# Kernel tuning notes

Measured on AMD Instinct MI355X. Metric: run time of the kernel, lower is better.

The kernel has to match this reference:

```python
import jax, jax.numpy as jnp
import numpy as np

B, C, H, W = 32, 512, 32, 32
D = C // 8

def setup_inputs() -> dict:
    key = jax.random.key(0)
    ks = jax.random.split(key, 5)
    return {
        "x": jax.random.normal(ks[0], (B, C, H, W), dtype=jnp.float32),
        "w1": jax.random.normal(ks[1], (D, C), dtype=jnp.float32) * (1.0 / np.sqrt(C)),
        "b1": jax.random.normal(ks[2], (D,), dtype=jnp.float32) * 0.01,
        "w2": jax.random.normal(ks[3], (C, C), dtype=jnp.float32) * (1.0 / np.sqrt(C)),
        "b2": jax.random.normal(ks[4], (C,), dtype=jnp.float32) * 0.01,
    }

def reference(x, w1, b1, w2, b2):
    b, c, h, w = x.shape
    n = h * w
    xf = x.reshape(b, c, n)                                   # [B,C,N]
    # 1x1 convs == channel-mixing GEMMs; conv1 is shared for q and k
    qk = jnp.einsum('bcn,dc->bdn', xf, w1) + b1[None, :, None]  # [B,D,N]
    v = jnp.einsum('bcn,oc->bon', xf, w2) + b2[None, :, None]   # [B,C,N]
    q = qk.transpose(0, 2, 1)                                 # [B,N,D]
    attn = jax.nn.softmax(jnp.einsum('bnd,bdm->bnm', q, qk), axis=-1)  # [B,N,N]
    out = jnp.einsum('bnm,bcm->bnc', attn, v)                 # [B,N,C]
    # Faithful quirk: original views [B,N,C] directly as [B,C,H,W] (no transpose)
    return x + out.reshape(b, c, h, w)
```

## Files before the change

### kernel.cpp

```cpp
#include <hip/hip_runtime.h>
#include <hip/hip_bf16.h>
#include <math.h>

#define B_ 32
#define C_ 512
#define N_ 1024
#define D_ 64
#define OPAD 640

typedef __attribute__((ext_vector_type(4))) float f32x4;
typedef __attribute__((ext_vector_type(4))) float float4v;
typedef __attribute__((ext_vector_type(8))) __bf16 bf16x8;

#define MFMA16(a, b, c) __builtin_amdgcn_mfma_f32_16x16x32_bf16((a), (b), (c), 0, 0, 0)

__device__ inline void load_lds16(const void* g, void* l) {
    __builtin_amdgcn_global_load_lds(
        (const __attribute__((address_space(1))) void*)g,
        (__attribute__((address_space(3))) void*)l, 16, 0, 0);
}

__global__ __launch_bounds__(256) void k_transpose_cast(
        const float* __restrict__ x,
        const float* __restrict__ w1, const float* __restrict__ w2,
        __hip_bfloat16* __restrict__ xT, __hip_bfloat16* __restrict__ Wbf) {
    __shared__ float tile[64][68];
    int b = blockIdx.z;
    int n0 = blockIdx.x * 64;
    int c0 = blockIdx.y * 64;
    int t = threadIdx.x;

    int lid = blockIdx.x + 16 * blockIdx.y + 128 * blockIdx.z;
    if (lid < 160) {
        int base = lid * 2048 + t * 8;
        int m = base >> 9, k = base & 511;
        alignas(16) __hip_bfloat16 wtmp[8];
        if (m < D_ + C_) {
            const float* s = (m < D_) ? w1 + (size_t)m * C_ + k
                                      : w2 + (size_t)(m - D_) * C_ + k;
            float4v a = *(const float4v*)s;
            float4v c = *(const float4v*)(s + 4);
            wtmp[0] = __float2bfloat16(a.x); wtmp[1] = __float2bfloat16(a.y);
            wtmp[2] = __float2bfloat16(a.z); wtmp[3] = __float2bfloat16(a.w);
            wtmp[4] = __float2bfloat16(c.x); wtmp[5] = __float2bfloat16(c.y);
            wtmp[6] = __float2bfloat16(c.z); wtmp[7] = __float2bfloat16(c.w);
        } else {
#pragma unroll
            for (int j = 0; j < 8; j++) wtmp[j] = __float2bfloat16(0.0f);
        }
        *(bf16x8*)(Wbf + base) = *(bf16x8*)wtmp;
    }

    const float* xb = x + (size_t)b * (C_ * N_);
#pragma unroll
    for (int i = 0; i < 4; i++) {
        int c = i * 16 + (t >> 4);
        int nc = (t & 15) * 4;
        *(float4v*)&tile[c][nc] =
            *(const float4v*)(xb + (size_t)(c0 + c) * N_ + n0 + nc);
    }
    __syncthreads();
    __hip_bfloat16* xTb = xT + (size_t)b * (N_ * C_);
#pragma unroll
    for (int i = 0; i < 2; i++) {
        int n = i * 32 + (t >> 3);
        int cs = (t & 7) * 8;
        alignas(16) __hip_bfloat16 tmp[8];
#pragma unroll
        for (int j = 0; j < 8; j++)
            tmp[j] = __float2bfloat16(tile[cs + j][n]);
        *(bf16x8*)(xTb + (size_t)(n0 + n) * C_ + c0 + cs) = *(bf16x8*)tmp;
    }
}

__global__ __launch_bounds__(256) void k_gemm_qkv(
        const __hip_bfloat16* __restrict__ Wbf,
        const __hip_bfloat16* __restrict__ xT,
        const float* __restrict__ b1, const float* __restrict__ b2,
        __hip_bfloat16* __restrict__ qkT, __hip_bfloat16* __restrict__ v) {
    __shared__ __hip_bfloat16 AB[2][2][128 * 64];
    __hip_bfloat16* epi = &AB[0][0][0];
    int b = blockIdx.x;
    int t = threadIdx.x;
    int wave = t >> 6, lane = t & 63, lr = lane & 15, quad = lane >> 4;
    int wm = wave >> 1, wn = wave & 1;
    int m_blk = blockIdx.z * 128;
    int n_blk = blockIdx.y * 128;
    const __hip_bfloat16* xTb = xT + (size_t)b * (N_ * C_);

#pragma unroll
    for (int i = 0; i < 4; i++) {
        int id = i * 256 + t;
        int r = id >> 3, cx = id & 7, gc = cx ^ (r & 7);
        load_lds16(Wbf + (size_t)(m_blk + r) * C_ + gc * 8, &AB[0][0][id * 8]);
        load_lds16(xTb + (size_t)(n_blk + r) * C_ + gc * 8, &AB[0][1][id * 8]);
    }
    __syncthreads();

    f32x4 acc[4][4] = {};
    for (int tt = 0; tt < 8; tt++) {
        const __hip_bfloat16* As = AB[tt & 1][0];
        const __hip_bfloat16* Bs = AB[tt & 1][1];
        if (tt < 7) {
            int kk = (tt + 1) * 64;
            __hip_bfloat16* An = AB[(tt + 1) & 1][0];
            __hip_bfloat16* Bn = AB[(tt + 1) & 1][1];
#pragma unroll
            for (int i = 0; i < 4; i++) {
                int id = i * 256 + t;
                int r = id >> 3, cx = id & 7, gc = cx ^ (r & 7);
                load_lds16(Wbf + (size_t)(m_blk + r) * C_ + kk + gc * 8, &An[id * 8]);
                load_lds16(xTb + (size_t)(n_blk + r) * C_ + kk + gc * 8, &Bn[id * 8]);
            }
        }
#pragma unroll
        for (int h = 0; h < 2; h++) {
            bf16x8 af[4], bfr[4];
#pragma unroll
            for (int i = 0; i < 4; i++) {
                int ra = wm * 64 + i * 16 + lr;
                int rb = wn * 64 + i * 16 + lr;
                int q = h * 4 + quad;
                af[i]  = *(const bf16x8*)&As[ra * 64 + (q ^ (lr & 7)) * 8];
                bfr[i] = *(const bf16x8*)&Bs[rb * 64 + (q ^ (lr & 7)) * 8];
            }
#pragma unroll
            for (int mt = 0; mt < 4; mt++)
#pragma unroll
                for (int nt = 0; nt < 4; nt++)
                    acc[mt][nt] = MFMA16(af[mt], bfr[nt], acc[mt][nt]);
        }
        __syncthreads();
    }

#pragma unroll
    for (int mt = 0; mt < 4; mt++) {
        int m_frag = m_blk + wm * 64 + mt * 16;
        if (m_frag >= D_ + C_) continue;
        int m0 = m_frag + quad * 4;
        if (m_frag < D_) {
#pragma unroll
            for (int nt = 0; nt < 4; nt++) {
                int n = n_blk + wn * 64 + nt * 16 + lr;
                alignas(8) __hip_bfloat16 tmp[4];
#pragma unroll
                for (int r = 0; r < 4; r++)
                    tmp[r] = __float2bfloat16(acc[mt][nt][r] + b1[m0 + r]);
                *reinterpret_cast<short4*>(qkT + ((size_t)b * N_ + n) * D_ + m0) =
                    *reinterpret_cast<short4*>(tmp);
            }
        } else {
#pragma unroll
            for (int nt = 0; nt < 4; nt++) {
#pragma unroll
                for (int r = 0; r < 4; r++) {
                    int c = m0 - D_ + r;
                    epi[(wave * 16 + quad * 4 + r) * 72 + nt * 16 + lr] =
                        __float2bfloat16(acc[mt][nt][r] + b2[c]);
                }
            }
            int cbase = m_frag - D_;
            int row = lane >> 2;
#pragma unroll
            for (int it = 0; it < 2; it++) {
                int col = it * 32 + (lane & 3) * 8;
                bf16x8 frag = *(const bf16x8*)&epi[(wave * 16 + row) * 72 + col];
                *(bf16x8*)(v + (size_t)(b * C_ + cbase + row) * N_
                             + n_blk + wn * 64 + col) = frag;
            }
        }
    }
}

__global__ __launch_bounds__(512, 2) void k_fused_attn(
        const __hip_bfloat16* __restrict__ qkT,
        const __hip_bfloat16* __restrict__ v,
        const float* __restrict__ x, float* __restrict__ out) {
    __shared__ char smem[67072];
    __hip_bfloat16* Ks0 = (__hip_bfloat16*)smem;
    __hip_bfloat16* Ks1 = (__hip_bfloat16*)(smem + 8192);
    __hip_bfloat16* Ps0 = (__hip_bfloat16*)(smem + 16384);
    __hip_bfloat16* Ps1 = (__hip_bfloat16*)(smem + 49152);
    float* Obuf = (float*)smem;
    __shared__ float Rs[128];

    int b = blockIdx.x;
    int t = threadIdx.x;
    int wave = t >> 6, lane = t & 63, lr = lane & 15, quad = lane >> 4;
    int wm = wave >> 2, wn = wave & 3;
    int n_blk = blockIdx.y * 128;
    const __hip_bfloat16* qb = qkT + (size_t)b * (N_ * D_);
    const __hip_bfloat16* vb = v + (size_t)b * (C_ * N_);

    {
        int r = t >> 3, cxx = t & 7, gc = cxx ^ (r & 7);
        load_lds16(qb + (size_t)r * D_ + gc * 8, &Ks0[t * 8]);
    }

    union bfu { bf16x8 v; __hip_bfloat16 h[8]; };
    bf16x8 bq[2];
    float shift;
    {
        int nq = n_blk + wave * 16 + lr;
        bq[0] = *(const bf16x8*)(qb + (size_t)nq * D_ + quad * 8);
        bq[1] = *(const bf16x8*)(qb + (size_t)nq * D_ + 32 + quad * 8);
        float sq = 0.f;
#pragma unroll
        for (int dh = 0; dh < 2; dh++) {
            bfu u; u.v = bq[dh];
#pragma unroll
            for (int j = 0; j < 8; j++) {
                float qv = __bfloat162float(u.h[j]);
                sq += qv * qv;
            }
        }
        sq += __shfl_xor(sq, 16);
        sq += __shfl_xor(sq, 32);
        shift = sq;
    }

    f32x4 acc[4][8] = {};
    float rsum = 0.f;

    __syncthreads();

    for (int tt = 0; tt < 16; ++tt) {
        const int kk = tt * 64;
        __hip_bfloat16* Kst = (tt & 1) ? Ks1 : Ks0;
        __hip_bfloat16* Ksn = (tt & 1) ? Ks0 : Ks1;
        __hip_bfloat16* Pst = (tt & 1) ? Ps1 : Ps0;

        if (tt < 15) {
            int r = t >> 3, cxx = t & 7, gc = cxx ^ (r & 7);
            load_lds16(qb + (size_t)(kk + 64 + r) * D_ + gc * 8, &Ksn[t * 8]);
        }

#pragma unroll
        for (int mi = 0; mi < 4; mi++) {
            int m = mi * 16 + lr;
            bf16x8 ak0 = *(const bf16x8*)&Kst[m * 64 + ((quad) ^ (lr & 7)) * 8];
            bf16x8 ak1 = *(const bf16x8*)&Kst[m * 64 + ((4 + quad) ^ (lr & 7)) * 8];
            f32x4 s = {};
            s = MFMA16(ak0, bq[0], s);
            s = MFMA16(ak1, bq[1], s);
            alignas(8) __hip_bfloat16 tmp[4];
#pragma unroll
            for (int r = 0; r < 4; r++) {
                float e = __expf(s[r] - shift);
                rsum += e;
                tmp[r] = __float2bfloat16(e);
            }
            int n = wave * 16 + lr;
            int cx2 = mi * 2 + (quad >> 1);
            int slot = cx2 ^ (lr & 7);
            *(short4*)&Pst[n * 64 + slot * 8 + (quad & 1) * 4] = *(short4*)tmp;
        }

        __syncthreads();

#pragma unroll
        for (int h = 0; h < 2; h++) {
            bf16x8 af[4];
#pragma unroll
            for (int i = 0; i < 4; i++) {
                int ra = wm * 64 + i * 16 + lr;
                af[i] = *(const bf16x8*)&Pst[ra * 64 + ((h * 4 + quad) ^ (lr & 7)) * 8];
            }
#pragma unroll
            for (int g = 0; g < 2; g++) {
                bf16x8 bfr[4];
#pragma unroll
                for (int j = 0; j < 4; j++) {
                    int rb = wn * 128 + (g * 4 + j) * 16 + lr;
                    bfr[j] = *(const bf16x8*)(vb + (size_t)rb * N_ + kk
                                              + (h * 4 + quad) * 8);
                }
#pragma unroll
                for (int mt = 0; mt < 4; mt++)
#pragma unroll
                    for (int j = 0; j < 4; j++)
                        acc[mt][g * 4 + j] = MFMA16(af[mt], bfr[j], acc[mt][g * 4 + j]);
            }
        }
    }

    rsum += __shfl_xor(rsum, 16);
    rsum += __shfl_xor(rsum, 32);
    if (quad == 0) Rs[wave * 16 + lr] = 1.0f / rsum;

    const float* xb = x + (size_t)b * (N_ * C_);
    float* ob = out + (size_t)b * (N_ * C_);
#pragma unroll
    for (int h = 0; h < 2; h++) {
#pragma unroll
        for (int g = 0; g < 2; g++) {
            __syncthreads();
            if (wm == h && (wn >> 1) == g) {
#pragma unroll
                for (int mt = 0; mt < 4; mt++)
#pragma unroll
                    for (int nt = 0; nt < 8; nt++)
#pragma unroll
                        for (int r = 0; r < 4; r++)
                            Obuf[(mt * 16 + quad * 4 + r) * 260
                                 + (wn & 1) * 128 + nt * 16 + lr] =
                                acc[mt][nt][r];
            }
            __syncthreads();
#pragma unroll
            for (int i = 0; i < 8; i++) {
                int id = i * 512 + t;
                int rl = id >> 6;
                int c4 = (id & 63) * 4;
                int n = n_blk + h * 64 + rl;
                float ri = Rs[h * 64 + rl];
                float4v o = *(const float4v*)&Obuf[rl * 260 + c4];
                size_t gidx = (size_t)n * C_ + g * 256 + c4;
                float4v xv = *(const float4v*)(xb + gidx);
                float4v res;
                res.x = xv.x + ri * o.x;
                res.y = xv.y + ri * o.y;
                res.z = xv.z + ri * o.z;
                res.w = xv.w + ri * o.w;
                *(float4v*)(ob + gidx) = res;
            }
        }
    }
}

extern "C" void kernel_launch(void* const* d_in, const int* in_sizes, int n_in,
                              void* d_out, int out_size, void* d_ws, size_t ws_size,
                              hipStream_t stream) {
    const float* x  = (const float*)d_in[0];
    const float* w1 = (const float*)d_in[1];
    const float* b1 = (const float*)d_in[2];
    const float* w2 = (const float*)d_in[3];
    const float* b2 = (const float*)d_in[4];
    float* out = (float*)d_out;

    char* ws = (char*)d_ws;
    size_t off = 0;
    __hip_bfloat16* Wbf = (__hip_bfloat16*)(ws + off); off += (size_t)OPAD * C_ * 2;
    __hip_bfloat16* xT  = (__hip_bfloat16*)(ws + off); off += (size_t)B_ * N_ * C_ * 2;
    __hip_bfloat16* qkT = (__hip_bfloat16*)(ws + off); off += (size_t)B_ * N_ * D_ * 2;
    __hip_bfloat16* v   = (__hip_bfloat16*)(ws + off); off += (size_t)B_ * C_ * N_ * 2;

    hipLaunchKernelGGL(k_transpose_cast, dim3(N_ / 64, C_ / 64, B_), dim3(256), 0, stream,
                       x, w1, w2, xT, Wbf);
    hipLaunchKernelGGL(k_gemm_qkv, dim3(B_, N_ / 128, OPAD / 128), dim3(256), 0, stream,
                       Wbf, xT, b1, b2, qkT, v);
    hipLaunchKernelGGL(k_fused_attn, dim3(B_, N_ / 128), dim3(512), 0, stream,
                       qkT, v, x, out);
}
```

Before: 241.3 us.

## Stage V tiles in double-buffered LDS and single-buffer K and P tiles

V tiles, previously read straight from global memory inside the PV MFMA loop, are now copied asynchronously into double-buffered swizzled LDS one iteration ahead. K and P become single-buffered, with the K prefetch issued after the barrier. The max-shift is folded into the MFMA accumulator initialisation, and setprio is raised around the PV MFMA block. LDS use grows to about 152KB, which limits occupancy to one block per CU despite launch_bounds(512,2), and each iteration now needs two barriers.

After: 199.8 us. 1.21x faster.

```diff
diff --git a/kernel.cpp b/kernel.cpp
--- a/kernel.cpp
+++ b/kernel.cpp
@@ -176,13 +176,13 @@
         const __hip_bfloat16* __restrict__ qkT,
         const __hip_bfloat16* __restrict__ v,
         const float* __restrict__ x, float* __restrict__ out) {
-    __shared__ char smem[67072];
-    __hip_bfloat16* Ks0 = (__hip_bfloat16*)smem;
-    __hip_bfloat16* Ks1 = (__hip_bfloat16*)(smem + 8192);
-    __hip_bfloat16* Ps0 = (__hip_bfloat16*)(smem + 16384);
-    __hip_bfloat16* Ps1 = (__hip_bfloat16*)(smem + 49152);
+    __shared__ char smem[155648];
+    __hip_bfloat16* Ks  = (__hip_bfloat16*)smem;
+    __hip_bfloat16* Vs0 = (__hip_bfloat16*)(smem + 8192);
+    __hip_bfloat16* Vs1 = (__hip_bfloat16*)(smem + 73728);
+    __hip_bfloat16* Ps  = (__hip_bfloat16*)(smem + 139264);
     float* Obuf = (float*)smem;
-    __shared__ float Rs[128];
+    float* Rs   = (float*)(smem + 66560);
 
     int b = blockIdx.x;
     int t = threadIdx.x;
@@ -194,12 +194,18 @@
 
     {
         int r = t >> 3, cxx = t & 7, gc = cxx ^ (r & 7);
-        load_lds16(qb + (size_t)r * D_ + gc * 8, &Ks0[t * 8]);
+        load_lds16(qb + (size_t)r * D_ + gc * 8, &Ks[t * 8]);
+    }
+#pragma unroll
+    for (int i = 0; i < 8; i++) {
+        int id = i * 512 + t;
+        int r = id >> 3, cxx = id & 7, gc = cxx ^ (r & 7);
+        load_lds16(vb + (size_t)r * N_ + gc * 8, &Vs0[id * 8]);
     }
 
     union bfu { bf16x8 v; __hip_bfloat16 h[8]; };
     bf16x8 bq[2];
-    float shift;
+    float nshift;
     {
         int nq = n_blk + wave * 16 + lr;
         bq[0] = *(const bf16x8*)(qb + (size_t)nq * D_ + quad * 8);
@@ -216,7 +222,7 @@
         }
         sq += __shfl_xor(sq, 16);
         sq += __shfl_xor(sq, 32);
-        shift = sq;
+        nshift = -sq;
     }
 
     f32x4 acc[4][8] = {};
@@ -225,46 +231,57 @@
     __syncthreads();
 
     for (int tt = 0; tt < 16; ++tt) {
-        const int kk = tt * 64;
-        __hip_bfloat16* Kst = (tt & 1) ? Ks1 : Ks0;
-        __hip_bfloat16* Ksn = (tt & 1) ? Ks0 : Ks1;
-        __hip_bfloat16* Pst = (tt & 1) ? Ps1 : Ps0;
+        int kk = tt * 64;
+        __hip_bfloat16* Vcur = (tt & 1) ? Vs1 : Vs0;
+        __hip_bfloat16* Vnxt = (tt & 1) ? Vs0 : Vs1;
 
         if (tt < 15) {
-            int r = t >> 3, cxx = t & 7, gc = cxx ^ (r & 7);
-            load_lds16(qb + (size_t)(kk + 64 + r) * D_ + gc * 8, &Ksn[t * 8]);
+#pragma unroll
+            for (int i = 0; i < 8; i++) {
+                int id = i * 512 + t;
+                int r = id >> 3, cxx = id & 7, gc = cxx ^ (r & 7);
+                load_lds16(vb + (size_t)r * N_ + kk + 64 + gc * 8, &Vnxt[id * 8]);
+            }
         }
 
 #pragma unroll
         for (int mi = 0; mi < 4; mi++) {
             int m = mi * 16 + lr;
-            bf16x8 ak0 = *(const bf16x8*)&Kst[m * 64 + ((quad) ^ (lr & 7)) * 8];
-            bf16x8 ak1 = *(const bf16x8*)&Kst[m * 64 + ((4 + quad) ^ (lr & 7)) * 8];
-            f32x4 s = {};
+            bf16x8 ak0 = *(const bf16x8*)&Ks[m * 64 + ((quad) ^ (lr & 7)) * 8];
+            bf16x8 ak1 = *(const bf16x8*)&Ks[m * 64 + ((4 + quad) ^ (lr & 7)) * 8];
+            f32x4 s = {nshift, nshift, nshift, nshift};
             s = MFMA16(ak0, bq[0], s);
             s = MFMA16(ak1, bq[1], s);
             alignas(8) __hip_bfloat16 tmp[4];
 #pragma unroll
             for (int r = 0; r < 4; r++) {
-                float e = __expf(s[r] - shift);
+                float e = __expf(s[r]);
                 rsum += e;
                 tmp[r] = __float2bfloat16(e);
             }
             int n = wave * 16 + lr;
             int cx2 = mi * 2 + (quad >> 1);
             int slot = cx2 ^ (lr & 7);
-            *(short4*)&Pst[n * 64 + slot * 8 + (quad & 1) * 4] = *(short4*)tmp;
-        }
-
-        __syncthreads();
-
+            *(short4*)&Ps[n * 64 + slot * 8 + (quad & 1) * 4] = *(short4*)tmp;
+        }
+
+        asm volatile("s_waitcnt lgkmcnt(0)" ::: "memory");
+        __builtin_amdgcn_s_barrier();
+        __builtin_amdgcn_sched_barrier(0);
+
+        if (tt < 15) {
+            int r = t >> 3, cxx = t & 7, gc = cxx ^ (r & 7);
+            load_lds16(qb + (size_t)(kk + 64 + r) * D_ + gc * 8, &Ks[t * 8]);
+        }
+
+        __builtin_amdgcn_s_setprio(1);
 #pragma unroll
         for (int h = 0; h < 2; h++) {
             bf16x8 af[4];
 #pragma unroll
             for (int i = 0; i < 4; i++) {
                 int ra = wm * 64 + i * 16 + lr;
-                af[i] = *(const bf16x8*)&Pst[ra * 64 + ((h * 4 + quad) ^ (lr & 7)) * 8];
+                af[i] = *(const bf16x8*)&Ps[ra * 64 + ((h * 4 + quad) ^ (lr & 7)) * 8];
             }
 #pragma unroll
             for (int g = 0; g < 2; g++) {
@@ -272,8 +289,7 @@
 #pragma unroll
                 for (int j = 0; j < 4; j++) {
                     int rb = wn * 128 + (g * 4 + j) * 16 + lr;
-                    bfr[j] = *(const bf16x8*)(vb + (size_t)rb * N_ + kk
-                                              + (h * 4 + quad) * 8);
+                    bfr[j] = *(const bf16x8*)&Vcur[rb * 64 + ((h * 4 + quad) ^ (lr & 7)) * 8];
                 }
 #pragma unroll
                 for (int mt = 0; mt < 4; mt++)
@@ -282,6 +298,8 @@
                         acc[mt][g * 4 + j] = MFMA16(af[mt], bfr[j], acc[mt][g * 4 + j]);
             }
         }
+        __builtin_amdgcn_s_setprio(0);
+        __syncthreads();
     }
 
     rsum += __shfl_xor(rsum, 16);
```
